# Kernel optimization log

Hardware: AMD Instinct MI355X
Metric: run time of the kernel (lower is better)

Reference implementation:

```python
import jax, jax.numpy as jnp
import numpy as np

B, S, D_IN, D_OUT = 4, 2048, 2048, 2048
E, R = 8, 8
SCALING = 16.0 / 8.0  # lora_alpha / r
# Dropout (p=0.05) treated as identity (eval mode) for a deterministic reference.

def setup_inputs() -> dict:
    key = jax.random.key(0)
    ks = jax.random.split(key, 8)
    x = jax.random.normal(ks[0], (B, S, D_IN), dtype=jnp.float32)
    base_W = jax.random.normal(ks[1], (D_OUT, D_IN), dtype=jnp.float32) * 0.02
    base_b = jax.random.normal(ks[2], (D_OUT,), dtype=jnp.float32) * 0.02
    shared_A = jax.random.normal(ks[3], (R, D_IN), dtype=jnp.float32) * 0.01
    shared_B = jax.random.normal(ks[4], (D_OUT, R), dtype=jnp.float32) * 0.01
    expert_A = jax.random.normal(ks[5], (E, R, D_IN), dtype=jnp.float32) * 0.01
    expert_B = jax.random.normal(ks[6], (E, D_OUT, R), dtype=jnp.float32) * 0.01
    task_emb = jax.random.normal(ks[7], (E, D_IN), dtype=jnp.float32) * 0.01
    collab_w = jnp.array(0.5, dtype=jnp.float32)
    return {"x": x, "base_W": base_W, "base_b": base_b,
            "shared_A": shared_A, "shared_B": shared_B,
            "expert_A": expert_A, "expert_B": expert_B,
            "task_emb": task_emb, "collab_w": collab_w}

def reference(x, base_W, base_b, shared_A, shared_B, expert_A, expert_B, task_emb, collab_w):
    # base linear: [B,S,D_out]
    base_out = jnp.einsum('bsi,oi->bso', x, base_W) + base_b
    # shared LoRA path
    shared_out = jnp.einsum('bsr,or->bso', jnp.einsum('bsi,ri->bsr', x, shared_A), shared_B) * SCALING
    # soft routing over task experts (task_id=None branch)
    x_mean = x.mean(axis=1)                               # [B,D_in]
    routing = jax.nn.softmax(x_mean @ task_emb.T, axis=-1)  # [B,E]
    t = jnp.einsum('bsi,eri->bser', x, expert_A)          # [B,S,E,R] low-rank
    task_out = jnp.einsum('bser,eor,be->bso', t, expert_B, routing) * SCALING
    cw = jax.nn.sigmoid(collab_w)
    return base_out + cw * shared_out + (1.0 - cw) * task_out
```

## Files before the change

kernel.cpp:

```cpp
#include <hip/hip_runtime.h>
#include <hip/hip_bf16.h>
#include <math.h>

#define BATCH 4
#define SEQ   2048
#define DIN   2048
#define DOUT  2048
#define NEXP  8
#define RANK  8
#define MTOT  (BATCH * SEQ)
#define KE    64
#define NKC   8

typedef __bf16 bf16x8 __attribute__((ext_vector_type(8)));
typedef __bf16 bf16x4 __attribute__((ext_vector_type(4)));
typedef float  f32x4  __attribute__((ext_vector_type(4)));

#define GLOBAL_AS __attribute__((address_space(1)))
#define LDS_AS    __attribute__((address_space(3)))

__global__ __launch_bounds__(256) void mega_prep(
    const float* __restrict__ x, const float* __restrict__ W,
    const float* __restrict__ expert_A, const float* __restrict__ shared_A,
    const float* __restrict__ expert_B, const float* __restrict__ shared_B,
    const float* __restrict__ task_emb, const float* __restrict__ collab,
    __bf16* __restrict__ xb, __bf16* __restrict__ Wb,
    __bf16* __restrict__ caug, __bf16* __restrict__ pt, float* __restrict__ plog)
{
    const int bid = blockIdx.x;
    const int t = threadIdx.x;

    if (bid >= 512) {
        if (bid < 4608) {
            size_t idx = ((size_t)(bid - 512) * 256 + t) * 4;
            int o = (int)(idx >> 11), i = (int)(idx & 2047);
            float cw = 1.0f / (1.0f + expf(-collab[0]));
            float s = cw * 2.0f;
            float4 w = *(const float4*)&W[idx];
            float dx = 0.f, dy = 0.f, dz = 0.f, dw = 0.f;
            #pragma unroll
            for (int r = 0; r < 8; ++r) {
                float bs = shared_B[(size_t)o * RANK + r];
                float4 as = *(const float4*)&shared_A[(size_t)r * DIN + i];
                dx += bs * as.x; dy += bs * as.y; dz += bs * as.z; dw += bs * as.w;
            }
            bf16x4 h = { (__bf16)(w.x + s * dx), (__bf16)(w.y + s * dy),
                         (__bf16)(w.z + s * dz), (__bf16)(w.w + s * dw) };
            *(bf16x4*)&Wb[idx] = h;
        } else {
            int idx = ((bid - 4608) * 256 + t) * 4;
            int o = idx >> 6, k = idx & 63;
            float cw = 1.0f / (1.0f + expf(-collab[0]));
            float s = (1.0f - cw) * 2.0f;
            float4 v = *(const float4*)&expert_B[((size_t)(k >> 3) * DOUT + o) * RANK + (k & 7)];
            bf16x4 h = { (__bf16)(s * v.x), (__bf16)(s * v.y),
                         (__bf16)(s * v.z), (__bf16)(s * v.w) };
            *(bf16x4*)&caug[idx] = h;
        }
        return;
    }

    __shared__ __bf16 lsA[128 * 64];
    __shared__ __bf16 lsB[96 * 64];
    __shared__ float lsc[32];
    const int lane = t & 63;
    const int w = t >> 6;
    const int kc = bid & 7;
    const int m0 = (bid >> 3) * 128;

    f32x4 acc[2][5];
    #pragma unroll
    for (int a = 0; a < 2; ++a)
        #pragma unroll
        for (int c = 0; c < 5; ++c) acc[a][c] = (f32x4){0.f, 0.f, 0.f, 0.f};

    for (int it = 0; it < 4; ++it) {
        int k0 = kc * 256 + it * 64;
        #pragma unroll
        for (int q = 0; q < 4; ++q) {
            int row = q * 32 + (t >> 3), sl = t & 7, seg = sl ^ (row & 7);
            const float* gp = x + (size_t)(m0 + row) * DIN + k0 + seg * 8;
            float4 v0 = *(const float4*)gp;
            float4 v1 = *(const float4*)(gp + 4);
            bf16x8 h = { (__bf16)v0.x, (__bf16)v0.y, (__bf16)v0.z, (__bf16)v0.w,
                         (__bf16)v1.x, (__bf16)v1.y, (__bf16)v1.z, (__bf16)v1.w };
            *(bf16x8*)&lsA[row * 64 + sl * 8] = h;
            *(bf16x8*)&xb[(size_t)(m0 + row) * DIN + k0 + seg * 8] = h;
        }
        #pragma unroll
        for (int q = 0; q < 3; ++q) {
            int c = q * 256 + t;
            int row = c >> 3, sl = c & 7, seg = sl ^ (row & 7);
            bf16x8 h = { (__bf16)0.f, (__bf16)0.f, (__bf16)0.f, (__bf16)0.f,
                         (__bf16)0.f, (__bf16)0.f, (__bf16)0.f, (__bf16)0.f };
            if (row < 64) {
                const float* gp = expert_A + (size_t)row * DIN + k0 + seg * 8;
                float4 v0 = *(const float4*)gp, v1 = *(const float4*)(gp + 4);
                h = bf16x8{ (__bf16)v0.x, (__bf16)v0.y, (__bf16)v0.z, (__bf16)v0.w,
                            (__bf16)v1.x, (__bf16)v1.y, (__bf16)v1.z, (__bf16)v1.w };
            } else if (row < 72) {
                const float* gp = task_emb + (size_t)(row - 64) * DIN + k0 + seg * 8;
                float4 v0 = *(const float4*)gp, v1 = *(const float4*)(gp + 4);
                h = bf16x8{ (__bf16)v0.x, (__bf16)v0.y, (__bf16)v0.z, (__bf16)v0.w,
                            (__bf16)v1.x, (__bf16)v1.y, (__bf16)v1.z, (__bf16)v1.w };
            }
            *(bf16x8*)&lsB[row * 64 + sl * 8] = h;
        }
        __syncthreads();
        #pragma unroll
        for (int kk = 0; kk < 2; ++kk) {
            bf16x8 af[2], bfr[5];
            #pragma unroll
            for (int tm = 0; tm < 2; ++tm) {
                int r = w * 32 + tm * 16 + (lane & 15);
                int slot = (kk * 4 + (lane >> 4)) ^ (r & 7);
                af[tm] = *(const bf16x8*)&lsA[r * 64 + slot * 8];
            }
            #pragma unroll
            for (int tn = 0; tn < 5; ++tn) {
                int r = tn * 16 + (lane & 15);
                int slot = (kk * 4 + (lane >> 4)) ^ (r & 7);
                bfr[tn] = *(const bf16x8*)&lsB[r * 64 + slot * 8];
            }
            #pragma unroll
            for (int tm = 0; tm < 2; ++tm)
                #pragma unroll
                for (int tn = 0; tn < 5; ++tn)
                    acc[tm][tn] = __builtin_amdgcn_mfma_f32_16x16x32_bf16(
                        af[tm], bfr[tn], acc[tm][tn], 0, 0, 0);
        }
        __syncthreads();
    }

    #pragma unroll
    for (int tm = 0; tm < 2; ++tm)
        #pragma unroll
        for (int tn = 0; tn < 4; ++tn) {
            int col = tn * 16 + (lane & 15);
            #pragma unroll
            for (int v = 0; v < 4; ++v) {
                int row = m0 + w * 32 + tm * 16 + (lane >> 4) * 4 + v;
                pt[((size_t)kc * MTOT + row) * KE + col] = (__bf16)acc[tm][tn][v];
            }
        }

    float s = 0.f;
    #pragma unroll
    for (int tm = 0; tm < 2; ++tm)
        #pragma unroll
        for (int v = 0; v < 4; ++v) s += acc[tm][4][v];
    s += __shfl_down(s, 32);
    s += __shfl_down(s, 16);
    if (lane < 8) lsc[w * 8 + lane] = s;
    __syncthreads();
    if (t < 8)
        plog[bid * 8 + t] = lsc[t] + lsc[8 + t] + lsc[16 + t] + lsc[24 + t];
}

__global__ __launch_bounds__(256) void gemm_main(
    const __bf16* __restrict__ xb, const __bf16* __restrict__ Wb,
    const __bf16* __restrict__ pt, const __bf16* __restrict__ caug,
    const float* __restrict__ plog, const float* __restrict__ bias,
    float* __restrict__ out)
{
    __shared__ __bf16 lsA[128 * 64];
    __shared__ __bf16 lsB[128 * 64];
    __shared__ float scr[32 * 8];
    __shared__ float lgs[NEXP];
    const int t = threadIdx.x;
    const int lane = t & 63;
    const int wm = (t >> 6) >> 1, wn = (t >> 6) & 1;
    const int m0 = blockIdx.x * 128;
    const int n0 = blockIdx.y * 128;
    const int b  = m0 >> 11;

    int rowq[4], segq[4], ldso[4];
    #pragma unroll
    for (int q = 0; q < 4; ++q) {
        rowq[q] = q * 32 + (t >> 3);
        segq[q] = (t & 7) ^ (rowq[q] & 7);
        ldso[q] = (q * 256 + (t & ~63)) * 8;
    }
    const __bf16* pA[4]; const __bf16* pB[4];
    #pragma unroll
    for (int q = 0; q < 4; ++q) {
        pA[q] = xb + (size_t)(m0 + rowq[q]) * DIN + segq[q] * 8;
        pB[q] = Wb + (size_t)(n0 + rowq[q]) * DIN + segq[q] * 8;
    }
    int aoff[2][4], boff[2][4];
    #pragma unroll
    for (int tm = 0; tm < 4; ++tm) {
        int r = wm * 64 + tm * 16 + (lane & 15);
        #pragma unroll
        for (int kk = 0; kk < 2; ++kk)
            aoff[kk][tm] = r * 64 + (((kk * 4 + (lane >> 4)) ^ (r & 7)) * 8);
    }
    #pragma unroll
    for (int tn = 0; tn < 4; ++tn) {
        int r = wn * 64 + tn * 16 + (lane & 15);
        #pragma unroll
        for (int kk = 0; kk < 2; ++kk)
            boff[kk][tn] = r * 64 + (((kk * 4 + (lane >> 4)) ^ (r & 7)) * 8);
    }

    f32x4 acc[4][4];
    #pragma unroll
    for (int a = 0; a < 4; ++a)
        #pragma unroll
        for (int c = 0; c < 4; ++c) acc[a][c] = (f32x4){0.f, 0.f, 0.f, 0.f};

    for (int it = 0; it < 32; ++it) {
        #pragma unroll
        for (int q = 0; q < 4; ++q) {
            __builtin_amdgcn_global_load_lds((GLOBAL_AS void*)pA[q],
                (LDS_AS void*)&lsA[ldso[q]], 16, 0, 0);
            __builtin_amdgcn_global_load_lds((GLOBAL_AS void*)pB[q],
                (LDS_AS void*)&lsB[ldso[q]], 16, 0, 0);
            pA[q] += 64; pB[q] += 64;
        }
        __syncthreads();
        #pragma unroll
        for (int kk = 0; kk < 2; ++kk) {
            bf16x8 af[4], bfr[4];
            #pragma unroll
            for (int tm = 0; tm < 4; ++tm) af[tm]  = *(const bf16x8*)&lsA[aoff[kk][tm]];
            #pragma unroll
            for (int tn = 0; tn < 4; ++tn) bfr[tn] = *(const bf16x8*)&lsB[boff[kk][tn]];
            #pragma unroll
            for (int tm = 0; tm < 4; ++tm)
                #pragma unroll
                for (int tn = 0; tn < 4; ++tn)
                    acc[tm][tn] = __builtin_amdgcn_mfma_f32_16x16x32_bf16(
                        af[tm], bfr[tn], acc[tm][tn], 0, 0, 0);
        }
        __syncthreads();
    }

    #pragma unroll
    for (int q = 0; q < 4; ++q) {
        const __bf16* qB = caug + (size_t)(n0 + rowq[q]) * KE + segq[q] * 8;
        __builtin_amdgcn_global_load_lds((GLOBAL_AS void*)qB,
            (LDS_AS void*)&lsB[ldso[q]], 16, 0, 0);
    }
    {
        const float* pb = plog + (size_t)b * 128 * 8;
        int e = t & 7, rr = t >> 3;
        float part = 0.f;
        #pragma unroll
        for (int j = 0; j < 4; ++j) part += pb[(rr + 32 * j) * 8 + e];
        scr[rr * 8 + e] = part;
    }
    __syncthreads();
    if (t < 8) {
        float s = 0.f;
        #pragma unroll
        for (int i = 0; i < 32; ++i) s += scr[i * 8 + t];
        lgs[t] = s;
    }
    __syncthreads();
    float f[NEXP];
    {
        float li[NEXP];
        #pragma unroll
        for (int e = 0; e < NEXP; ++e) li[e] = lgs[e] * (1.0f / (float)SEQ);
        float mx = li[0];
        #pragma unroll
        for (int e = 1; e < NEXP; ++e) mx = fmaxf(mx, li[e]);
        float den = 0.f;
        #pragma unroll
        for (int e = 0; e < NEXP; ++e) { f[e] = expf(li[e] - mx); den += f[e]; }
        float rden = 1.0f / den;
        #pragma unroll
        for (int e = 0; e < NEXP; ++e) f[e] *= rden;
    }
    #pragma unroll
    for (int q = 0; q < 4; ++q) {
        int row = rowq[q], seg = segq[q];
        const __bf16* p0 = pt + (size_t)(m0 + row) * KE + seg * 8;
        float sum[8] = {0.f,0.f,0.f,0.f,0.f,0.f,0.f,0.f};
        #pragma unroll
        for (int kc = 0; kc < NKC; ++kc) {
            bf16x8 v = *(const bf16x8*)(p0 + (size_t)kc * MTOT * KE);
            #pragma unroll
            for (int j = 0; j < 8; ++j) sum[j] += (float)v[j];
        }
        float fe = f[seg];
        bf16x8 h;
        #pragma unroll
        for (int j = 0; j < 8; ++j) h[j] = (__bf16)(sum[j] * fe);
        *(bf16x8*)&lsA[row * 64 + (t & 7) * 8] = h;
    }
    __syncthreads();
    #pragma unroll
    for (int kk = 0; kk < 2; ++kk) {
        bf16x8 af[4], bfr[4];
        #pragma unroll
        for (int tm = 0; tm < 4; ++tm) af[tm]  = *(const bf16x8*)&lsA[aoff[kk][tm]];
        #pragma unroll
        for (int tn = 0; tn < 4; ++tn) bfr[tn] = *(const bf16x8*)&lsB[boff[kk][tn]];
        #pragma unroll
        for (int tm = 0; tm < 4; ++tm)
            #pragma unroll
            for (int tn = 0; tn < 4; ++tn)
                acc[tm][tn] = __builtin_amdgcn_mfma_f32_16x16x32_bf16(
                    af[tm], bfr[tn], acc[tm][tn], 0, 0, 0);
    }

    #pragma unroll
    for (int tm = 0; tm < 4; ++tm)
        #pragma unroll
        for (int tn = 0; tn < 4; ++tn) {
            int col = n0 + wn * 64 + tn * 16 + (lane & 15);
            float bv = bias[col];
            #pragma unroll
            for (int v = 0; v < 4; ++v) {
                int row = m0 + wm * 64 + tm * 16 + (lane >> 4) * 4 + v;
                out[(size_t)row * DOUT + col] = acc[tm][tn][v] + bv;
            }
        }
}

extern "C" void kernel_launch(void* const* d_in, const int* in_sizes, int n_in,
                              void* d_out, int out_size, void* d_ws, size_t ws_size,
                              hipStream_t stream)
{
    const float* x        = (const float*)d_in[0];
    const float* base_W   = (const float*)d_in[1];
    const float* base_b   = (const float*)d_in[2];
    const float* shared_A = (const float*)d_in[3];
    const float* shared_B = (const float*)d_in[4];
    const float* expert_A = (const float*)d_in[5];
    const float* expert_B = (const float*)d_in[6];
    const float* task_emb = (const float*)d_in[7];
    const float* collab_w = (const float*)d_in[8];
    float* out = (float*)d_out;

    char* ws = (char*)d_ws;
    __bf16* xb   = (__bf16*)(ws + 0);
    __bf16* Wb   = (__bf16*)(ws + 33554432);
    __bf16* pt   = (__bf16*)(ws + 41943040);
    __bf16* caug = (__bf16*)(ws + 50331648);
    float*  plog = (float*) (ws + 50593792);

    mega_prep<<<dim3(4736), 256, 0, stream>>>(x, base_W, expert_A, shared_A,
                                              expert_B, shared_B, task_emb, collab_w,
                                              xb, Wb, caug, pt, plog);
    gemm_main<<<dim3(64, 16), 256, 0, stream>>>(xb, Wb, pt, caug, plog, base_b, out);
}
```

Measured before the change: 233.9 us.

## Retile main GEMM to 256x256 blocks with double-buffered LDS prefetch

Replaces the 128x128 tile, 4-wave GEMM with a 256x256 tile, 8-wave version that double-buffers the K slices in LDS. The next slice is prefetched with direct global-to-LDS loads while the current one feeds MFMA, and raw s_barrier plus setprio interleave the waves. The intent is to hide global load latency and raise data reuse per byte loaded. The cost is a large LDS footprint (about one block per CU), many accumulator registers, and hand-managed waitcnt ordering that is easy to get wrong.

```diff
diff --git a/kernel.cpp b/kernel.cpp
--- a/kernel.cpp
+++ b/kernel.cpp
@@ -18,6 +18,8 @@
 
 #define GLOBAL_AS __attribute__((address_space(1)))
 #define LDS_AS    __attribute__((address_space(3)))
+
+#define BARRIER() asm volatile("s_barrier" ::: "memory")
 
 __global__ __launch_bounds__(256) void mega_prep(
     const float* __restrict__ x, const float* __restrict__ W,
@@ -157,107 +159,127 @@
         plog[bid * 8 + t] = lsc[t] + lsc[8 + t] + lsc[16 + t] + lsc[24 + t];
 }
 
-__global__ __launch_bounds__(256) void gemm_main(
+__global__ __launch_bounds__(512, 2) void gemm_main(
     const __bf16* __restrict__ xb, const __bf16* __restrict__ Wb,
     const __bf16* __restrict__ pt, const __bf16* __restrict__ caug,
     const float* __restrict__ plog, const float* __restrict__ bias,
     float* __restrict__ out)
 {
-    __shared__ __bf16 lsA[128 * 64];
-    __shared__ __bf16 lsB[128 * 64];
-    __shared__ float scr[32 * 8];
-    __shared__ float lgs[NEXP];
+    __shared__ __bf16 lds[65536];
     const int t = threadIdx.x;
     const int lane = t & 63;
-    const int wm = (t >> 6) >> 1, wn = (t >> 6) & 1;
-    const int m0 = blockIdx.x * 128;
-    const int n0 = blockIdx.y * 128;
+    const int wid = t >> 6;
+    const int wm = wid >> 2, wn = wid & 3;
+    const int bid = blockIdx.x;
+    const int n0 = (bid & 7) * 256;
+    const int m0 = (bid >> 3) * 256;
     const int b  = m0 >> 11;
 
-    int rowq[4], segq[4], ldso[4];
+    const int srow = t >> 3;
+    const int sseg = (t & 7) ^ (srow & 7);
+    const __bf16* gA = xb + (size_t)(m0 + srow) * DIN + sseg * 8;
+    const __bf16* gB = Wb + (size_t)(n0 + srow) * DIN + sseg * 8;
+    const int lbase = (t & ~63) * 8;
+
+    int aoff[8], boff[4];
+    #pragma unroll
+    for (int fm = 0; fm < 8; ++fm) {
+        int r = wm * 128 + fm * 16 + (lane & 15);
+        aoff[fm] = r * 64 + (((lane >> 4) ^ (r & 7)) * 8);
+    }
+    #pragma unroll
+    for (int fn = 0; fn < 4; ++fn) {
+        int r = wn * 64 + fn * 16 + (lane & 15);
+        boff[fn] = r * 64 + (((lane >> 4) ^ (r & 7)) * 8);
+    }
+
+    f32x4 acc[8][4];
+    #pragma unroll
+    for (int i = 0; i < 8; ++i)
+        #pragma unroll
+        for (int j = 0; j < 4; ++j) acc[i][j] = (f32x4){0.f, 0.f, 0.f, 0.f};
+
     #pragma unroll
     for (int q = 0; q < 4; ++q) {
-        rowq[q] = q * 32 + (t >> 3);
-        segq[q] = (t & 7) ^ (rowq[q] & 7);
-        ldso[q] = (q * 256 + (t & ~63)) * 8;
-    }
-    const __bf16* pA[4]; const __bf16* pB[4];
-    #pragma unroll
-    for (int q = 0; q < 4; ++q) {
-        pA[q] = xb + (size_t)(m0 + rowq[q]) * DIN + segq[q] * 8;
-        pB[q] = Wb + (size_t)(n0 + rowq[q]) * DIN + segq[q] * 8;
-    }
-    int aoff[2][4], boff[2][4];
-    #pragma unroll
-    for (int tm = 0; tm < 4; ++tm) {
-        int r = wm * 64 + tm * 16 + (lane & 15);
-        #pragma unroll
-        for (int kk = 0; kk < 2; ++kk)
-            aoff[kk][tm] = r * 64 + (((kk * 4 + (lane >> 4)) ^ (r & 7)) * 8);
-    }
-    #pragma unroll
-    for (int tn = 0; tn < 4; ++tn) {
-        int r = wn * 64 + tn * 16 + (lane & 15);
-        #pragma unroll
-        for (int kk = 0; kk < 2; ++kk)
-            boff[kk][tn] = r * 64 + (((kk * 4 + (lane >> 4)) ^ (r & 7)) * 8);
-    }
-
-    f32x4 acc[4][4];
-    #pragma unroll
-    for (int a = 0; a < 4; ++a)
-        #pragma unroll
-        for (int c = 0; c < 4; ++c) acc[a][c] = (f32x4){0.f, 0.f, 0.f, 0.f};
-
-    for (int it = 0; it < 32; ++it) {
-        #pragma unroll
-        for (int q = 0; q < 4; ++q) {
-            __builtin_amdgcn_global_load_lds((GLOBAL_AS void*)pA[q],
-                (LDS_AS void*)&lsA[ldso[q]], 16, 0, 0);
-            __builtin_amdgcn_global_load_lds((GLOBAL_AS void*)pB[q],
-                (LDS_AS void*)&lsB[ldso[q]], 16, 0, 0);
-            pA[q] += 64; pB[q] += 64;
-        }
-        __syncthreads();
-        #pragma unroll
-        for (int kk = 0; kk < 2; ++kk) {
-            bf16x8 af[4], bfr[4];
-            #pragma unroll
-            for (int tm = 0; tm < 4; ++tm) af[tm]  = *(const bf16x8*)&lsA[aoff[kk][tm]];
-            #pragma unroll
-            for (int tn = 0; tn < 4; ++tn) bfr[tn] = *(const bf16x8*)&lsB[boff[kk][tn]];
-            #pragma unroll
-            for (int tm = 0; tm < 4; ++tm)
+        __builtin_amdgcn_global_load_lds((GLOBAL_AS void*)(gA + q * 64 * DIN),
+            (LDS_AS void*)&lds[q * 4096 + lbase], 16, 0, 0);
+        __builtin_amdgcn_global_load_lds((GLOBAL_AS void*)(gB + q * 64 * DIN),
+            (LDS_AS void*)&lds[32768 + q * 4096 + lbase], 16, 0, 0);
+    }
+    asm volatile("s_waitcnt vmcnt(0)" ::: "memory");
+    BARRIER();
+
+    for (int kt = 0; kt < 32; ++kt) {
+        const int abase = (kt & 1) * 16384;
+        const int bbase = 32768 + (kt & 1) * 16384;
+        if (kt < 31) {
+            const int nb = ((kt & 1) ^ 1) * 16384;
+            const __bf16* a2 = gA + (kt + 1) * 64;
+            const __bf16* b2 = gB + (kt + 1) * 64;
+            #pragma unroll
+            for (int q = 0; q < 4; ++q) {
+                __builtin_amdgcn_global_load_lds((GLOBAL_AS void*)(a2 + q * 64 * DIN),
+                    (LDS_AS void*)&lds[nb + q * 4096 + lbase], 16, 0, 0);
+                __builtin_amdgcn_global_load_lds((GLOBAL_AS void*)(b2 + q * 64 * DIN),
+                    (LDS_AS void*)&lds[32768 + nb + q * 4096 + lbase], 16, 0, 0);
+            }
+        }
+        bf16x8 bfrag[4][2];
+        #pragma unroll
+        for (int fn = 0; fn < 4; ++fn) {
+            bfrag[fn][0] = *(const bf16x8*)&lds[bbase + boff[fn]];
+            bfrag[fn][1] = *(const bf16x8*)&lds[bbase + (boff[fn] ^ 32)];
+        }
+        #pragma unroll
+        for (int p = 0; p < 4; ++p) {
+            bf16x8 afr[2][2];
+            #pragma unroll
+            for (int i = 0; i < 2; ++i) {
+                int fm = p * 2 + i;
+                afr[i][0] = *(const bf16x8*)&lds[abase + aoff[fm]];
+                afr[i][1] = *(const bf16x8*)&lds[abase + (aoff[fm] ^ 32)];
+            }
+            BARRIER();
+            __builtin_amdgcn_s_setprio(1);
+            #pragma unroll
+            for (int kk = 0; kk < 2; ++kk)
                 #pragma unroll
-                for (int tn = 0; tn < 4; ++tn)
-                    acc[tm][tn] = __builtin_amdgcn_mfma_f32_16x16x32_bf16(
-                        af[tm], bfr[tn], acc[tm][tn], 0, 0, 0);
-        }
-        __syncthreads();
-    }
-
-    #pragma unroll
-    for (int q = 0; q < 4; ++q) {
-        const __bf16* qB = caug + (size_t)(n0 + rowq[q]) * KE + segq[q] * 8;
-        __builtin_amdgcn_global_load_lds((GLOBAL_AS void*)qB,
-            (LDS_AS void*)&lsB[ldso[q]], 16, 0, 0);
-    }
+                for (int i = 0; i < 2; ++i)
+                    #pragma unroll
+                    for (int fn = 0; fn < 4; ++fn)
+                        acc[p * 2 + i][fn] = __builtin_amdgcn_mfma_f32_16x16x32_bf16(
+                            afr[i][kk], bfrag[fn][kk], acc[p * 2 + i][fn], 0, 0, 0);
+            __builtin_amdgcn_s_setprio(0);
+            if (p == 3 && kt < 31)
+                asm volatile("s_waitcnt vmcnt(0)" ::: "memory");
+            BARRIER();
+        }
+    }
+
+    {
+        const __bf16* gC = caug + (size_t)(n0 + srow) * KE + sseg * 8;
+        #pragma unroll
+        for (int q = 0; q < 4; ++q)
+            __builtin_amdgcn_global_load_lds((GLOBAL_AS void*)(gC + q * 64 * KE),
+                (LDS_AS void*)&lds[32768 + q * 4096 + lbase], 16, 0, 0);
+    }
+    float* scr = (float*)&lds[16384];
+    float* lgs = scr + 512;
     {
         const float* pb = plog + (size_t)b * 128 * 8;
         int e = t & 7, rr = t >> 3;
-        float part = 0.f;
-        #pragma unroll
-        for (int j = 0; j < 4; ++j) part += pb[(rr + 32 * j) * 8 + e];
-        scr[rr * 8 + e] = part;
-    }
-    __syncthreads();
+        scr[rr * 8 + e] = pb[rr * 8 + e] + pb[(rr + 64) * 8 + e];
+    }
+    asm volatile("s_waitcnt lgkmcnt(0)" ::: "memory");
+    BARRIER();
     if (t < 8) {
         float s = 0.f;
         #pragma unroll
-        for (int i = 0; i < 32; ++i) s += scr[i * 8 + t];
+        for (int i = 0; i < 64; ++i) s += scr[i * 8 + t];
         lgs[t] = s;
     }
-    __syncthreads();
+    asm volatile("s_waitcnt lgkmcnt(0)" ::: "memory");
+    BARRIER();
     float f[NEXP];
     {
         float li[NEXP];
@@ -275,49 +297,56 @@
     }
     #pragma unroll
     for (int q = 0; q < 4; ++q) {
-        int row = rowq[q], seg = segq[q];
-        const __bf16* p0 = pt + (size_t)(m0 + row) * KE + seg * 8;
-        float sum[8] = {0.f,0.f,0.f,0.f,0.f,0.f,0.f,0.f};
+        int row = q * 64 + srow;
+        const __bf16* p0 = pt + (size_t)(m0 + row) * KE + sseg * 8;
+        float sum[8] = {0.f, 0.f, 0.f, 0.f, 0.f, 0.f, 0.f, 0.f};
         #pragma unroll
         for (int kc = 0; kc < NKC; ++kc) {
             bf16x8 v = *(const bf16x8*)(p0 + (size_t)kc * MTOT * KE);
             #pragma unroll
             for (int j = 0; j < 8; ++j) sum[j] += (float)v[j];
         }
-        float fe = f[seg];
+        float fe = f[sseg];
         bf16x8 h;
         #pragma unroll
         for (int j = 0; j < 8; ++j) h[j] = (__bf16)(sum[j] * fe);
-        *(bf16x8*)&lsA[row * 64 + (t & 7) * 8] = h;
-    }
-    __syncthreads();
-    #pragma unroll
-    for (int kk = 0; kk < 2; ++kk) {
-        bf16x8 af[4], bfr[4];
-        #pragma unroll
-        for (int tm = 0; tm < 4; ++tm) af[tm]  = *(const bf16x8*)&lsA[aoff[kk][tm]];
-        #pragma unroll
-        for (int tn = 0; tn < 4; ++tn) bfr[tn] = *(const bf16x8*)&lsB[boff[kk][tn]];
-        #pragma unroll
-        for (int tm = 0; tm < 4; ++tm)
-            #pragma unroll
-            for (int tn = 0; tn < 4; ++tn)
-                acc[tm][tn] = __builtin_amdgcn_mfma_f32_16x16x32_bf16(
-                    af[tm], bfr[tn], acc[tm][tn], 0, 0, 0);
-    }
-
-    #pragma unroll
-    for (int tm = 0; tm < 4; ++tm)
-        #pragma unroll
-        for (int tn = 0; tn < 4; ++tn) {
-            int col = n0 + wn * 64 + tn * 16 + (lane & 15);
-            float bv = bias[col];
-            #pragma unroll
-            for (int v = 0; v < 4; ++v) {
-                int row = m0 + wm * 64 + tm * 16 + (lane >> 4) * 4 + v;
-                out[(size_t)row * DOUT + col] = acc[tm][tn][v] + bv;
-            }
-        }
+        *(bf16x8*)&lds[row * 64 + (t & 7) * 8] = h;
+    }
+    asm volatile("s_waitcnt vmcnt(0) lgkmcnt(0)" ::: "memory");
+    BARRIER();
+    {
+        bf16x8 bfrag[4][2];
+        #pragma unroll
+        for (int fn = 0; fn < 4; ++fn) {
+            bfrag[fn][0] = *(const bf16x8*)&lds[32768 + boff[fn]];
+            bfrag[fn][1] = *(const bf16x8*)&lds[32768 + (boff[fn] ^ 32)];
+        }
+        #pragma unroll
+        for (int fm = 0; fm < 8; ++fm) {
+            bf16x8 a0 = *(const bf16x8*)&lds[aoff[fm]];
+            bf16x8 a1 = *(const bf16x8*)&lds[aoff[fm] ^ 32];
+            #pragma unroll
+            for (int fn = 0; fn < 4; ++fn) {
+                acc[fm][fn] = __builtin_amdgcn_mfma_f32_16x16x32_bf16(
+                    a0, bfrag[fn][0], acc[fm][fn], 0, 0, 0);
+                acc[fm][fn] = __builtin_amdgcn_mfma_f32_16x16x32_bf16(
+                    a1, bfrag[fn][1], acc[fm][fn], 0, 0, 0);
+            }
+        }
+    }
+
+    #pragma unroll
+    for (int fn = 0; fn < 4; ++fn) {
+        int col = n0 + wn * 64 + fn * 16 + (lane & 15);
+        float bv = bias[col];
+        #pragma unroll
+        for (int fm = 0; fm < 8; ++fm) {
+            int row = m0 + wm * 128 + fm * 16 + (lane >> 4) * 4;
+            #pragma unroll
+            for (int v = 0; v < 4; ++v)
+                out[(size_t)(row + v) * DOUT + col] = acc[fm][fn][v] + bv;
+        }
+    }
 }
 
 extern "C" void kernel_launch(void* const* d_in, const int* in_sizes, int n_in,
@@ -345,5 +374,5 @@
     mega_prep<<<dim3(4736), 256, 0, stream>>>(x, base_W, expert_A, shared_A,
                                               expert_B, shared_B, task_emb, collab_w,
                                               xb, Wb, caug, pt, plog);
-    gemm_main<<<dim3(64, 16), 256, 0, stream>>>(xb, Wb, pt, caug, plog, base_b, out);
+    gemm_main<<<dim3(256), 512, 0, stream>>>(xb, Wb, pt, caug, plog, base_b, out);
 }
```

Measured after the change: 237.7 us. No clear change (+1.6%).
